# Optimization experiments

Hardware: AMD Instinct MI355X
Metric: run time of the kernel (lower is better)

Reference implementation:

```python
import jax, jax.numpy as jnp
import numpy as np

B, T, D = 1, 512, 64
EPS = 1e-5
DT = 0.01  # uniform measurement spacing (t_equal == 1)


def setup_inputs() -> dict:
    key = jax.random.key(0)
    ks = jax.random.split(key, 12)
    f32 = jnp.float32
    inp = {
        'Z_q': jax.random.normal(ks[0], (B, 2, T, D), f32),
        'Z_k': jax.random.normal(ks[1], (B, 2, T, D), f32),
        'Z_v': jax.random.normal(ks[2], (B, 2, T, D), f32),
        't_measure_all': jnp.arange(T + 1, dtype=f32)[None, :] * DT,
        # shared linear projections W_q, W_k (Linear(input_dim -> d_k))
        'Wq_w': jax.random.normal(ks[3], (D, D), f32) / np.sqrt(D),
        'Wq_b': jnp.zeros((D,), f32),
        'Wk_w': jax.random.normal(ks[4], (D, D), f32) / np.sqrt(D),
        'Wk_b': jnp.zeros((D,), f32),
        # shared dynamics eigenvalues: (2, D/2, 1) = (real, imag) halves
        'lambda1': jax.random.normal(ks[5], (2, D // 2, 1), f32),
        # per-block noise params
        'lambda_Omega': jax.random.normal(ks[6], (D,), f32) / D,
        'lambda_Gamma': jax.random.normal(ks[7], (D,), f32) / D,
        'noise_floor': jnp.asarray(1.0, f32),
        'tau': jnp.asarray(1.0, f32),
        'nu': jnp.asarray(1.0, f32),
        'eta_param': jnp.zeros((D,), f32),
        'lambda_C': jnp.ones((D,), f32),
    }
    return inp


def _afa_forward(Z_q, Z_k, Z_v, t_measure_all, Wq_w, Wq_b, Wk_w, Wk_b,
                 lambda1, lambda_Omega, lambda_Gamma, noise_floor, tau, nu,
                 eta_param, lambda_C):
    # --- compute_lambda_h: conjugate-pair eigenvalues, stable (Re < 0) ---
    a_half = -jnp.abs(lambda1[0, :, 0])          # (D/2,) real parts
    b_half = lambda1[1, :, 0]                    # (D/2,) imag parts
    a = jnp.concatenate([a_half, a_half])        # (D,)
    b = jnp.concatenate([b_half, -b_half])       # (D,)
    lambda_h = jnp.stack([a, b])                 # (2, D)

    lOm = jnp.abs(lambda_Omega)                  # (D,)
    lGa = jnp.abs(lambda_Gamma) + EPS            # (D,)

    # --- projections (applied on last dim, per complex component) ---
    Q = jnp.einsum('bcti,oi->bcto', Z_q, Wq_w) + Wq_b   # (B,2,T,D)
    K = jnp.einsum('bcti,oi->bcto', Z_k, Wk_w) + Wk_b   # (B,2,T,D)
    V = Z_v                                             # (B,2,T,D)

    t = t_measure_all[:, :-1]                    # (B,T)
    dt_ij = (t[:, :, None] - t[:, None, :])[..., None]  # (B,T,T,1) = t_i - t_j

    # --- complex exponential kernel exp(lambda * (t_i - t_j)) ---
    e = jnp.exp(a * dt_ij)                       # (B,T,T,D)
    cs = jnp.cos(b * dt_ij)
    sn = jnp.sin(b * dt_ij)

    Kr, Ki = K[:, 0][:, None, :, :], K[:, 1][:, None, :, :]   # key at time j
    Vr, Vi = V[:, 0][:, None, :, :], V[:, 1][:, None, :, :]   # value at time j
    Qr, Qi = Q[:, 0][:, :, None, :], Q[:, 1][:, :, None, :]   # query at time i

    # propagated estimates z_hat_ij = exp(lambda*dt) * v_j  (complex)
    Zr = e * (cs * Vr - sn * Vi)
    Zi = e * (sn * Vr + cs * Vi)
    # residuals r_ij = q_i - exp(lambda*dt) * k_j
    Rr = Qr - e * (cs * Kr - sn * Ki)
    Ri = Qi - e * (sn * Kr + cs * Ki)

    # --- covariance kernel: accumulated process noise over |dt| ---
    abs_dt = jnp.abs(dt_ij)
    V_ij = lambda_C * lOm * (1.0 - jnp.exp(2.0 * a * abs_dt)) / (-2.0 * a + EPS)  # (B,T,T,D)

    # --- Mahalanobis-weighted attention scores ---
    mahal = (Rr * Rr + Ri * Ri) / (V_ij + lGa)                     # (B,T,T,D)
    dist_sum = jnp.abs(nu) * jnp.sum(mahal, axis=3, keepdims=True)  # (B,T,T,1)
    base = V_ij * (jnp.abs(noise_floor) + dist_sum)
    scores = -jnp.abs(tau) * jnp.log(base + EPS)                    # (B,T,T,D)

    causal = jnp.tril(jnp.ones((T, T), bool))                       # i >= j
    scores = jnp.where(causal[None, :, :, None], scores, -jnp.inf)
    Q_ij = jax.nn.softmax(scores, axis=2)                           # softmax over j

    Zhat = jnp.stack([Zr, Zi], axis=1) * causal[None, None, :, :, None]  # (B,2,T,T,D)
    est_v_avg = jnp.einsum('bijd,bcijd->bcid', Q_ij, Zhat)               # (B,2,T,D)

    eta = jax.nn.sigmoid(eta_param)                                 # (D,)
    est_latent = (1.0 - eta) * V + eta * est_v_avg                  # (B,2,T,D)

    # one-step forward propagator exp(lambda * (t_T - t_{T-1}))
    dT = t_measure_all[:, -1] - t_measure_all[:, -2]                # (B,)
    me = jnp.exp(a * dT[:, None])
    mat_exp = jnp.stack([me * jnp.cos(b * dT[:, None]),
                         me * jnp.sin(b * dT[:, None])], axis=1)    # (B,2,D)

    return est_latent, Q_ij, Zhat, lambda_h, mat_exp


def reference(Z_q, Z_k, Z_v, t_measure_all, Wq_w, Wq_b, Wk_w, Wk_b,
              lambda1, lambda_Omega, lambda_Gamma, noise_floor, tau, nu,
              eta_param, lambda_C):
    return _afa_forward(Z_q, Z_k, Z_v, t_measure_all, Wq_w, Wq_b, Wk_w, Wk_b,
                        lambda1, lambda_Omega, lambda_Gamma, noise_floor, tau,
                        nu, eta_param, lambda_C)
```

## Files before the change

### kernel.cpp

```cpp
#include <hip/hip_runtime.h>
#include <math.h>

#define TT 512
#define DD 64
#define EPSF 1e-5f

typedef float f4 __attribute__((ext_vector_type(4)));

#define O_EST  0
#define O_QIJ  (2*TT*DD)
#define O_ZHAT (O_QIJ + TT*TT*DD)
#define O_LH   (O_ZHAT + 2*TT*TT*DD)
#define O_ME   (O_LH + 2*DD)

#define W_QBUF 0
#define W_KBUF (W_QBUF + 2*TT*DD)
#define W_CA   (W_KBUF + 2*TT*DD)
#define W_CB   (W_CA + DD)
#define W_CC   (W_CB + DD)
#define W_CG   (W_CC + DD)

__device__ __forceinline__ unsigned int rne16(float x) {
    unsigned int u = __float_as_uint(x);
    return u + 0x7FFFu + ((u >> 16) & 1u);
}

__global__ __launch_bounds__(128) void afa_proj_kernel(
    const float* __restrict__ Zq, const float* __restrict__ Zk,
    const float* __restrict__ Wq_w, const float* __restrict__ Wq_b,
    const float* __restrict__ Wk_w, const float* __restrict__ Wk_b,
    const float* __restrict__ l1, const float* __restrict__ t_all,
    const float* __restrict__ lOm_, const float* __restrict__ lGa_,
    const float* __restrict__ lC,
    float* __restrict__ Qbuf, float* __restrict__ Kbuf,
    float* __restrict__ ws, float* __restrict__ out)
{
    int b = blockIdx.x;
    int c = b / TT, t = b % TT;
    __shared__ float zq[DD], zk[DD];
    int tid = threadIdx.x;
    if (tid < DD) zq[tid] = Zq[(c*TT + t)*DD + tid];
    else          zk[tid-DD] = Zk[(c*TT + t)*DD + (tid-DD)];
    __syncthreads();
    int o = tid & 63;
    const float* __restrict__ W  = (tid < 64) ? Wq_w : Wk_w;
    const float* __restrict__ bs = (tid < 64) ? Wq_b : Wk_b;
    const float* __restrict__ z  = (tid < 64) ? zq : zk;
    float* __restrict__ dst      = (tid < 64) ? Qbuf : Kbuf;
    float acc = bs[o];
    #pragma unroll
    for (int i4 = 0; i4 < 16; ++i4) {
        f4 w4 = *(const f4*)&W[o*DD + i4*4];
        acc = fmaf(z[i4*4+0], w4.x, acc);
        acc = fmaf(z[i4*4+1], w4.y, acc);
        acc = fmaf(z[i4*4+2], w4.z, acc);
        acc = fmaf(z[i4*4+3], w4.w, acc);
    }
    dst[(c*TT + t)*DD + o] = acc;

    if (b == 0 && tid < 64) {
        int d = tid;
        int h = d & 31;
        float a  = -fabsf(l1[h]);
        float bb = (d < 32) ? l1[32 + h] : -l1[32 + h];
        out[O_LH + d]      = a;
        out[O_LH + DD + d] = bb;
        float dT = t_all[TT] - t_all[TT-1];
        float me = __expf(a * dT);
        out[O_ME + d]      = me * __cosf(bb * dT);
        out[O_ME + DD + d] = me * __sinf(bb * dT);
        ws[W_CA + d] = a;
        ws[W_CB + d] = bb;
        ws[W_CC + d] = lC[d] * fabsf(lOm_[d]) / (-2.0f * a + EPSF);
        ws[W_CG + d] = fabsf(lGa_[d]) + EPSF;
    }
}

__global__ __launch_bounds__(512, 4) void afa_row2_kernel(
    const float* __restrict__ Zv, const float* __restrict__ t_all,
    const float* __restrict__ nf,  const float* __restrict__ tau_,
    const float* __restrict__ nu_, const float* __restrict__ etap,
    const float* __restrict__ ws, float* __restrict__ out)
{
    const float* Qbuf = ws + W_QBUF;
    const float* Kbuf = ws + W_KBUF;

    int b = blockIdx.x;
    int i = (b < 256) ? b : (767 - b);
    int tid = threadIdx.x;
    int w  = tid >> 6;
    int l  = tid & 63;
    int jg = l >> 4;
    int d0 = (l & 15) * 4;

    __shared__ float t_lds[TT];
    __shared__ unsigned int pP[TT*DD/2];
    __shared__ float lsS[8][DD], lsR[8][DD], lsI[8][DD];

    t_lds[tid] = t_all[tid];

    f4 A4 = *(const f4*)&ws[W_CA + d0];
    f4 B4 = *(const f4*)&ws[W_CB + d0];
    f4 C4 = *(const f4*)&ws[W_CC + d0];
    f4 G4 = *(const f4*)&ws[W_CG + d0];
    const float* A = (const float*)&A4;
    const float* B = (const float*)&B4;
    const float* C = (const float*)&C4;
    const float* G = (const float*)&G4;
    float noise = fabsf(nf[0]);
    float tau_a = fabsf(tau_[0]);
    float nu_a  = fabsf(nu_[0]);
    float ti = t_all[i];
    f4 QR4 = *(const f4*)&Qbuf[i*DD + d0];
    f4 QI4 = *(const f4*)&Qbuf[TT*DD + i*DD + d0];
    const float* QR = (const float*)&QR4;
    const float* QI = (const float*)&QI4;

    float* __restrict__ Qout  = out + O_QIJ  + (size_t)i*TT*DD;
    float* __restrict__ Z0out = out + O_ZHAT + (size_t)i*TT*DD;
    float* __restrict__ Z1out = out + O_ZHAT + (size_t)TT*TT*DD + (size_t)i*TT*DD;

    f4 zz4 = (f4)(0.0f);

    __syncthreads();

    float s[4]  = {0.f,0.f,0.f,0.f};
    float ar[4] = {0.f,0.f,0.f,0.f};
    float ai[4] = {0.f,0.f,0.f,0.f};
    for (int it = 0; it < 16; ++it) {
        int j = it*32 + w*4 + jg;
        unsigned int* __restrict__ pw = &pP[(j*DD + d0) >> 1];
        if (j <= i) {
            float dt = ti - t_lds[j];
            f4 KR4 = *(const f4*)&Kbuf[j*DD + d0];
            f4 KI4 = *(const f4*)&Kbuf[TT*DD + j*DD + d0];
            f4 VR4 = *(const f4*)&Zv[j*DD + d0];
            f4 VI4 = *(const f4*)&Zv[TT*DD + j*DD + d0];
            const float* KR = (const float*)&KR4;
            const float* KI = (const float*)&KI4;
            const float* VR = (const float*)&VR4;
            const float* VI = (const float*)&VI4;
            float e[4], cs[4], sn[4], ZR[4], ZI[4], Vij[4];
            float mah = 0.f;
            #pragma unroll
            for (int k = 0; k < 4; ++k) {
                e[k]  = __expf(A[k] * dt);
                float ang = B[k] * dt;
                cs[k] = __cosf(ang); sn[k] = __sinf(ang);
                ZR[k] = e[k] * (cs[k]*VR[k] - sn[k]*VI[k]);
                ZI[k] = e[k] * (sn[k]*VR[k] + cs[k]*VI[k]);
            }
            f4 z0, z1;
            float* Z0 = (float*)&z0;
            float* Z1 = (float*)&z1;
            #pragma unroll
            for (int k = 0; k < 4; ++k) { Z0[k] = ZR[k]; Z1[k] = ZI[k]; }
            *(f4*)&Z0out[(size_t)j*DD + d0] = z0;
            *(f4*)&Z1out[(size_t)j*DD + d0] = z1;
            #pragma unroll
            for (int k = 0; k < 4; ++k) {
                float Rr = QR[k] - e[k] * (cs[k]*KR[k] - sn[k]*KI[k]);
                float Ri = QI[k] - e[k] * (sn[k]*KR[k] + cs[k]*KI[k]);
                Vij[k] = C[k] * (1.0f - e[k]*e[k]);
                mah += (Rr*Rr + Ri*Ri) / (Vij[k] + G[k]);
            }
            mah += __shfl_xor(mah, 1);
            mah += __shfl_xor(mah, 2);
            mah += __shfl_xor(mah, 4);
            mah += __shfl_xor(mah, 8);
            float w1 = noise + nu_a * mah;
            float p[4];
            #pragma unroll
            for (int k = 0; k < 4; ++k) {
                float base = Vij[k] * w1;
                float sc = -tau_a * __logf(base + EPSF);
                p[k] = __expf(sc);
                s[k]  += p[k];
                ar[k] = fmaf(p[k], ZR[k], ar[k]);
                ai[k] = fmaf(p[k], ZI[k], ai[k]);
            }
            pw[0] = (rne16(p[0]) >> 16) | (rne16(p[1]) & 0xFFFF0000u);
            pw[1] = (rne16(p[2]) >> 16) | (rne16(p[3]) & 0xFFFF0000u);
        } else {
            *(f4*)&Z0out[(size_t)j*DD + d0] = zz4;
            *(f4*)&Z1out[(size_t)j*DD + d0] = zz4;
            pw[0] = 0u; pw[1] = 0u;
        }
    }
    #pragma unroll
    for (int k = 0; k < 4; ++k) {
        s[k]  += __shfl_xor(s[k], 16);  s[k]  += __shfl_xor(s[k], 32);
        ar[k] += __shfl_xor(ar[k], 16); ar[k] += __shfl_xor(ar[k], 32);
        ai[k] += __shfl_xor(ai[k], 16); ai[k] += __shfl_xor(ai[k], 32);
    }
    if (jg == 0) {
        #pragma unroll
        for (int k = 0; k < 4; ++k) {
            lsS[w][d0+k] = s[k];
            lsR[w][d0+k] = ar[k];
            lsI[w][d0+k] = ai[k];
        }
    }
    __syncthreads();

    f4 S4 = (f4)(0.0f);
    #pragma unroll
    for (int ww = 0; ww < 8; ++ww) S4 += *(const f4*)&lsS[ww][d0];
    f4 inv4;
    inv4.x = 1.0f/S4.x; inv4.y = 1.0f/S4.y;
    inv4.z = 1.0f/S4.z; inv4.w = 1.0f/S4.w;
    const float* IV = (const float*)&inv4;
    if (tid < 64) {
        float S = 0.f, AR = 0.f, AI = 0.f;
        #pragma unroll
        for (int ww = 0; ww < 8; ++ww) {
            S += lsS[ww][tid]; AR += lsR[ww][tid]; AI += lsI[ww][tid];
        }
        float inv = 1.0f / S;
        float eta = 1.0f / (1.0f + __expf(-etap[tid]));
        float vr = Zv[i*DD + tid], vi = Zv[TT*DD + i*DD + tid];
        out[O_EST + i*DD + tid]         = (1.0f - eta)*vr + eta*AR*inv;
        out[O_EST + TT*DD + i*DD + tid] = (1.0f - eta)*vi + eta*AI*inv;
    }

    int jl = tid >> 4;
    for (int it = 0; it < 16; ++it) {
        int j = it*32 + jl;
        unsigned int p0 = pP[((j*DD + d0) >> 1) + 0];
        unsigned int p1 = pP[((j*DD + d0) >> 1) + 1];
        f4 q4;
        q4.x = __uint_as_float(p0 << 16)          * IV[0];
        q4.y = __uint_as_float(p0 & 0xFFFF0000u)  * IV[1];
        q4.z = __uint_as_float(p1 << 16)          * IV[2];
        q4.w = __uint_as_float(p1 & 0xFFFF0000u)  * IV[3];
        *(f4*)&Qout[(size_t)j*DD + d0] = q4;
    }
}

extern "C" void kernel_launch(void* const* d_in, const int* in_sizes, int n_in,
                              void* d_out, int out_size, void* d_ws, size_t ws_size,
                              hipStream_t stream) {
    const float* Zq    = (const float*)d_in[0];
    const float* Zk    = (const float*)d_in[1];
    const float* Zv    = (const float*)d_in[2];
    const float* t_all = (const float*)d_in[3];
    const float* Wq_w  = (const float*)d_in[4];
    const float* Wq_b  = (const float*)d_in[5];
    const float* Wk_w  = (const float*)d_in[6];
    const float* Wk_b  = (const float*)d_in[7];
    const float* l1    = (const float*)d_in[8];
    const float* lOm   = (const float*)d_in[9];
    const float* lGa   = (const float*)d_in[10];
    const float* nf    = (const float*)d_in[11];
    const float* tau   = (const float*)d_in[12];
    const float* nu    = (const float*)d_in[13];
    const float* etap  = (const float*)d_in[14];
    const float* lC    = (const float*)d_in[15];
    float* out = (float*)d_out;
    float* ws  = (float*)d_ws;

    afa_proj_kernel<<<2*TT, 128, 0, stream>>>(Zq, Zk, Wq_w, Wq_b, Wk_w, Wk_b,
                                              l1, t_all, lOm, lGa, lC,
                                              ws + W_QBUF, ws + W_KBUF, ws, out);
    afa_row2_kernel<<<TT, 512, 0, stream>>>(Zv, t_all, nf, tau, nu, etap,
                                            ws, out);
}
```

Baseline: 40.99 us.

## Split masked zero-fill into separate kernel and trim row loop to causal range

```diff
diff --git a/kernel.cpp b/kernel.cpp
--- a/kernel.cpp
+++ b/kernel.cpp
@@ -76,7 +76,23 @@
     }
 }
 
-__global__ __launch_bounds__(512, 4) void afa_row2_kernel(
+__global__ __launch_bounds__(256) void afa_zfill_kernel(float* __restrict__ out)
+{
+    int b = blockIdx.x;
+    int i = (b & 1) ? (TT - 1 - (b >> 1)) : (b >> 1);
+    int tid = threadIdx.x;
+    size_t row = (size_t)i*TT*DD + (size_t)(i+1)*DD;
+    int nz = (TT - 1 - i) * DD / 4;
+    f4 z = (f4)(0.0f);
+    f4* __restrict__ q  = (f4*)(out + O_QIJ  + row);
+    f4* __restrict__ z0 = (f4*)(out + O_ZHAT + row);
+    f4* __restrict__ z1 = (f4*)(out + O_ZHAT + (size_t)TT*TT*DD + row);
+    for (int k = tid; k < nz; k += 256) {
+        q[k] = z; z0[k] = z; z1[k] = z;
+    }
+}
+
+__global__ __launch_bounds__(512, 4) void afa_row3_kernel(
     const float* __restrict__ Zv, const float* __restrict__ t_all,
     const float* __restrict__ nf,  const float* __restrict__ tau_,
     const float* __restrict__ nu_, const float* __restrict__ etap,
@@ -120,16 +136,15 @@
     float* __restrict__ Z0out = out + O_ZHAT + (size_t)i*TT*DD;
     float* __restrict__ Z1out = out + O_ZHAT + (size_t)TT*TT*DD + (size_t)i*TT*DD;
 
-    f4 zz4 = (f4)(0.0f);
+    int nIt = (i >> 5) + 1;
 
     __syncthreads();
 
     float s[4]  = {0.f,0.f,0.f,0.f};
     float ar[4] = {0.f,0.f,0.f,0.f};
     float ai[4] = {0.f,0.f,0.f,0.f};
-    for (int it = 0; it < 16; ++it) {
+    for (int it = 0; it < nIt; ++it) {
         int j = it*32 + w*4 + jg;
-        unsigned int* __restrict__ pw = &pP[(j*DD + d0) >> 1];
         if (j <= i) {
             float dt = ti - t_lds[j];
             f4 KR4 = *(const f4*)&Kbuf[j*DD + d0];
@@ -179,12 +194,9 @@
                 ar[k] = fmaf(p[k], ZR[k], ar[k]);
                 ai[k] = fmaf(p[k], ZI[k], ai[k]);
             }
+            unsigned int* __restrict__ pw = &pP[(j*DD + d0) >> 1];
             pw[0] = (rne16(p[0]) >> 16) | (rne16(p[1]) & 0xFFFF0000u);
             pw[1] = (rne16(p[2]) >> 16) | (rne16(p[3]) & 0xFFFF0000u);
-        } else {
-            *(f4*)&Z0out[(size_t)j*DD + d0] = zz4;
-            *(f4*)&Z1out[(size_t)j*DD + d0] = zz4;
-            pw[0] = 0u; pw[1] = 0u;
         }
     }
     #pragma unroll
@@ -224,16 +236,18 @@
     }
 
     int jl = tid >> 4;
-    for (int it = 0; it < 16; ++it) {
+    for (int it = 0; it < nIt; ++it) {
         int j = it*32 + jl;
-        unsigned int p0 = pP[((j*DD + d0) >> 1) + 0];
-        unsigned int p1 = pP[((j*DD + d0) >> 1) + 1];
-        f4 q4;
-        q4.x = __uint_as_float(p0 << 16)          * IV[0];
-        q4.y = __uint_as_float(p0 & 0xFFFF0000u)  * IV[1];
-        q4.z = __uint_as_float(p1 << 16)          * IV[2];
-        q4.w = __uint_as_float(p1 & 0xFFFF0000u)  * IV[3];
-        *(f4*)&Qout[(size_t)j*DD + d0] = q4;
+        if (j <= i) {
+            unsigned int p0 = pP[((j*DD + d0) >> 1) + 0];
+            unsigned int p1 = pP[((j*DD + d0) >> 1) + 1];
+            f4 q4;
+            q4.x = __uint_as_float(p0 << 16)          * IV[0];
+            q4.y = __uint_as_float(p0 & 0xFFFF0000u)  * IV[1];
+            q4.z = __uint_as_float(p1 << 16)          * IV[2];
+            q4.w = __uint_as_float(p1 & 0xFFFF0000u)  * IV[3];
+            *(f4*)&Qout[(size_t)j*DD + d0] = q4;
+        }
     }
 }
 
@@ -262,6 +276,7 @@
     afa_proj_kernel<<<2*TT, 128, 0, stream>>>(Zq, Zk, Wq_w, Wq_b, Wk_w, Wk_b,
                                               l1, t_all, lOm, lGa, lC,
                                               ws + W_QBUF, ws + W_KBUF, ws, out);
-    afa_row2_kernel<<<TT, 512, 0, stream>>>(Zv, t_all, nf, tau, nu, etap,
+    afa_zfill_kernel<<<TT, 256, 0, stream>>>(out);
+    afa_row3_kernel<<<TT, 512, 0, stream>>>(Zv, t_all, nf, tau, nu, etap,
                                             ws, out);
 }
```

New measurement: 53.81 us. 1.31x slower.
